# Kernel optimization log

Measured on AMD Instinct MI355X. Metric: run time of the kernel, lower is better.

The kernel has to match this reference:

```python
import jax, jax.numpy as jnp
import numpy as np

N = 100000      # num nodes
E = 1600000     # num edges (avg degree 16)
F_IN = 256      # num_node_features
HID = 128       # hid_dim
C = 16          # num_classes


def gcn_conv(x, W, b, src, dst, num_nodes):
    # Linear transform first (PyG GCNConv transforms then aggregates)
    h = x @ W  # [N, out]
    # Symmetric normalization with self-loops already included in src/dst
    ones = jnp.ones_like(dst, dtype=h.dtype)
    deg = jax.ops.segment_sum(ones, dst, num_segments=num_nodes)  # in-degree incl. self-loop
    dinv = jnp.where(deg > 0, jax.lax.rsqrt(deg), 0.0)
    norm = dinv[src] * dinv[dst]                 # [E+N]
    msg = h[src] * norm[:, None]                 # gather + scale
    out = jax.ops.segment_sum(msg, dst, num_segments=num_nodes)  # scatter-add
    return out + b


def setup_inputs() -> dict:
    key = jax.random.key(0)
    k = jax.random.split(key, 4)
    x = jax.random.normal(k[0], (N, F_IN), dtype=jnp.float32)
    edge_index = jax.random.randint(k[1], (2, E), 0, N, dtype=jnp.int32)
    W1 = jax.random.normal(k[2], (F_IN, HID), dtype=jnp.float32) * (1.0 / np.sqrt(F_IN))
    b1 = jnp.zeros((HID,), dtype=jnp.float32)
    W2 = jax.random.normal(k[3], (HID, C), dtype=jnp.float32) * (1.0 / np.sqrt(HID))
    b2 = jnp.zeros((C,), dtype=jnp.float32)
    return {"x": x, "edge_index": edge_index, "W1": W1, "b1": b1, "W2": W2, "b2": b2}


def reference(x, edge_index, W1, b1, W2, b2):
    num_nodes = x.shape[0]
    loop = jnp.arange(num_nodes, dtype=edge_index.dtype)
    src = jnp.concatenate([edge_index[0], loop])  # add self-loops
    dst = jnp.concatenate([edge_index[1], loop])
    h = gcn_conv(x, W1, b1, src, dst, num_nodes)
    h = jax.nn.relu(h)
    # F.dropout(training=self.training): identity in eval mode
    out = gcn_conv(h, W2, b2, src, dst, num_nodes)
    return out
```

## Files before the change

kernel.cpp:

```cpp
#include <hip/hip_runtime.h>
#include <cstddef>

#define CAP 48
#define NBUILD 4096

typedef short short8 __attribute__((ext_vector_type(8)));
typedef float floatx4 __attribute__((ext_vector_type(4)));

__device__ inline float b2f_lo(unsigned int u) {
  union { unsigned int i; float f; } c;
  c.i = u << 16;
  return c.f;
}
__device__ inline float b2f_hi(unsigned int u) {
  union { unsigned int i; float f; } c;
  c.i = u & 0xFFFF0000u;
  return c.f;
}
__device__ inline unsigned short f2b(float f) {
  union { float f; unsigned int i; } c;
  c.f = f;
  unsigned int u = c.i;
  unsigned int r = (u + 0x7FFFu + ((u >> 16) & 1u)) >> 16;
  return (unsigned short)r;
}
__device__ inline float dinv_of(int c) { return rsqrtf((float)(c + 1)); }

__global__ void k_prep(int* __restrict__ cnt, int N,
                       const float* __restrict__ W1, unsigned short* __restrict__ W1T) {
  int i = blockIdx.x * 256 + threadIdx.x;
  if (i < N) cnt[i] = 0;
  if (i < 256 * 128) {
    int k = i >> 7, n = i & 127;
    W1T[n * 256 + k] = f2b(W1[i]);
  }
}

__global__ __launch_bounds__(256) void k_build_gemm1(
    const int* __restrict__ src, const int* __restrict__ dst, int E, int N,
    int* __restrict__ cnt, int* __restrict__ bucket,
    const float* __restrict__ X, const unsigned short* __restrict__ W1T,
    unsigned short* __restrict__ H1, int M) {
  __shared__ unsigned short As[64 * 72];
  __shared__ unsigned short Bs[128 * 72];

  if ((int)blockIdx.x < NBUILD) {
    const int g = blockIdx.x & 7;
    const int S = (N + 7) >> 3;
    const int lo = g * S;
    const int hi = min(N, lo + S);
    const int tb = ((int)blockIdx.x >> 3) * 256 + (int)threadIdx.x;
    const int T = (NBUILD >> 3) * 256;
    const int E4 = E & ~3;

    for (int i0 = tb * 4; i0 < E4; i0 += T * 4) {
      int4 d4 = *(const int4*)(dst + i0);
      int4 s4 = *(const int4*)(src + i0);
      int p0 = CAP, p1 = CAP, p2 = CAP, p3 = CAP;
      if (d4.x >= lo && d4.x < hi) p0 = atomicAdd(&cnt[d4.x], 1);
      if (d4.y >= lo && d4.y < hi) p1 = atomicAdd(&cnt[d4.y], 1);
      if (d4.z >= lo && d4.z < hi) p2 = atomicAdd(&cnt[d4.z], 1);
      if (d4.w >= lo && d4.w < hi) p3 = atomicAdd(&cnt[d4.w], 1);
      if (p0 < CAP) bucket[(size_t)d4.x * CAP + p0] = s4.x;
      if (p1 < CAP) bucket[(size_t)d4.y * CAP + p1] = s4.y;
      if (p2 < CAP) bucket[(size_t)d4.z * CAP + p2] = s4.z;
      if (p3 < CAP) bucket[(size_t)d4.w * CAP + p3] = s4.w;
    }
    if (tb < E - E4) {
      int i = E4 + tb;
      int d = dst[i], s = src[i];
      if (d >= lo && d < hi) {
        int pos = atomicAdd(&cnt[d], 1);
        if (pos < CAP) bucket[(size_t)d * CAP + pos] = s;
      }
    }
    return;
  }

  const int bid = (int)blockIdx.x - NBUILD;
  const int tid = threadIdx.x;
  const int wave = tid >> 6;
  const int lane = tid & 63;
  const int quad = lane >> 4;
  const int l16 = lane & 15;
  const int row0 = bid * 64;
  const int n0 = wave * 32;

  floatx4 acc[4][2];
#pragma unroll
  for (int r = 0; r < 4; r++)
#pragma unroll
    for (int c = 0; c < 2; c++) acc[r][c] = (floatx4){0.f, 0.f, 0.f, 0.f};

  for (int k0 = 0; k0 < 256; k0 += 64) {
    {
      int r = tid >> 2;
      int qk = (tid & 3) * 16;
      int gr = row0 + r;
      float4 v[4];
#pragma unroll
      for (int u = 0; u < 4; u++) v[u] = make_float4(0.f, 0.f, 0.f, 0.f);
      if (gr < M) {
        const float4* xp = (const float4*)(X + (size_t)gr * 256 + k0 + qk);
#pragma unroll
        for (int u = 0; u < 4; u++) v[u] = xp[u];
      }
      unsigned short tmp[16];
#pragma unroll
      for (int u = 0; u < 4; u++) {
        tmp[u * 4 + 0] = f2b(v[u].x); tmp[u * 4 + 1] = f2b(v[u].y);
        tmp[u * 4 + 2] = f2b(v[u].z); tmp[u * 4 + 3] = f2b(v[u].w);
      }
      unsigned short* p = As + r * 72 + qk;
      *(uint4*)(p) = *(const uint4*)(tmp);
      *(uint4*)(p + 8) = *(const uint4*)(tmp + 8);
    }
    {
      int n = tid >> 1;
      int half = (tid & 1) * 32;
      const uint4* wp = (const uint4*)(W1T + (size_t)n * 256 + k0 + half);
      uint4 w0 = wp[0];
      uint4 w1 = wp[1];
      uint4 w2 = wp[2];
      uint4 w3 = wp[3];
      unsigned short* p = Bs + n * 72 + half;
      *(uint4*)(p) = w0;
      *(uint4*)(p + 8) = w1;
      *(uint4*)(p + 16) = w2;
      *(uint4*)(p + 24) = w3;
    }
    __syncthreads();

#pragma unroll
    for (int s = 0; s < 2; s++) {
      short8 afr[4], bfr[2];
#pragma unroll
      for (int r = 0; r < 4; r++)
        afr[r] = *(const short8*)(As + (r * 16 + l16) * 72 + s * 32 + quad * 8);
#pragma unroll
      for (int c = 0; c < 2; c++)
        bfr[c] = *(const short8*)(Bs + (n0 + c * 16 + l16) * 72 + s * 32 + quad * 8);
#pragma unroll
      for (int r = 0; r < 4; r++)
#pragma unroll
        for (int c = 0; c < 2; c++)
          acc[r][c] = __builtin_amdgcn_mfma_f32_16x16x32_bf16(afr[r], bfr[c], acc[r][c], 0, 0, 0);
    }
    __syncthreads();
  }

#pragma unroll
  for (int r = 0; r < 4; r++) {
#pragma unroll
    for (int c = 0; c < 2; c++) {
      int col = n0 + c * 16 + l16;
#pragma unroll
      for (int i = 0; i < 4; i++) {
        int gr = row0 + r * 16 + quad * 4 + i;
        if (gr < M) H1[(size_t)gr * 128 + col] = f2b(acc[r][c][i]);
      }
    }
  }
}

__global__ __launch_bounds__(256) void k_agg1(const unsigned short* __restrict__ H1,
                                              const int* __restrict__ cnt,
                                              const int* __restrict__ bucket,
                                              const float* __restrict__ b1,
                                              unsigned short* __restrict__ A1, int N) {
  const int lane = threadIdx.x & 15;
  const int node = blockIdx.x * 16 + (threadIdx.x >> 4);
  if (node >= N) return;
  const int cn = cnt[node];
  const float di = dinv_of(cn);
  const float wself = di * di;
  const int deg = min(cn, CAP);
  const int* bk = bucket + (size_t)node * CAP;

  int idx0 = (lane < deg) ? bk[lane] : 0;
  int idx1 = (lane + 16 < deg) ? bk[lane + 16] : 0;
  int idx2 = (lane + 32 < deg) ? bk[lane + 32] : 0;
  float dv0 = (lane < deg) ? dinv_of(cnt[idx0]) : 0.f;
  float dv1 = (lane + 16 < deg) ? dinv_of(cnt[idx1]) : 0.f;
  float dv2 = (lane + 32 < deg) ? dinv_of(cnt[idx2]) : 0.f;

  uint4 hs = ((const uint4*)(H1 + (size_t)node * 128))[lane];
  float a0 = b2f_lo(hs.x) * wself, a1 = b2f_hi(hs.x) * wself;
  float a2 = b2f_lo(hs.y) * wself, a3 = b2f_hi(hs.y) * wself;
  float a4 = b2f_lo(hs.z) * wself, a5 = b2f_hi(hs.z) * wself;
  float a6 = b2f_lo(hs.w) * wself, a7 = b2f_hi(hs.w) * wself;
  float c0 = 0.f, c1 = 0.f, c2 = 0.f, c3 = 0.f, c4 = 0.f, c5 = 0.f, c6 = 0.f, c7 = 0.f;

  for (int j = 0; j < deg; j += 4) {
    int b = j >> 4;
    int idxB = (b == 0) ? idx0 : ((b == 1) ? idx1 : idx2);
    float dvB = (b == 0) ? dv0 : ((b == 1) ? dv1 : dv2);
    int base = j & 15;
    int s0 = __shfl(idxB, base + 0, 16);
    int s1 = __shfl(idxB, base + 1, 16);
    int s2 = __shfl(idxB, base + 2, 16);
    int s3 = __shfl(idxB, base + 3, 16);
    float w0 = __shfl(dvB, base + 0, 16) * di;
    float w1 = __shfl(dvB, base + 1, 16) * di;
    float w2 = __shfl(dvB, base + 2, 16) * di;
    float w3 = __shfl(dvB, base + 3, 16) * di;
    uint4 v0 = ((const uint4*)(H1 + (size_t)s0 * 128))[lane];
    uint4 v1 = ((const uint4*)(H1 + (size_t)s1 * 128))[lane];
    uint4 v2 = ((const uint4*)(H1 + (size_t)s2 * 128))[lane];
    uint4 v3 = ((const uint4*)(H1 + (size_t)s3 * 128))[lane];
    a0 += b2f_lo(v0.x) * w0; a1 += b2f_hi(v0.x) * w0;
    a2 += b2f_lo(v0.y) * w0; a3 += b2f_hi(v0.y) * w0;
    a4 += b2f_lo(v0.z) * w0; a5 += b2f_hi(v0.z) * w0;
    a6 += b2f_lo(v0.w) * w0; a7 += b2f_hi(v0.w) * w0;
    c0 += b2f_lo(v1.x) * w1; c1 += b2f_hi(v1.x) * w1;
    c2 += b2f_lo(v1.y) * w1; c3 += b2f_hi(v1.y) * w1;
    c4 += b2f_lo(v1.z) * w1; c5 += b2f_hi(v1.z) * w1;
    c6 += b2f_lo(v1.w) * w1; c7 += b2f_hi(v1.w) * w1;
    a0 += b2f_lo(v2.x) * w2; a1 += b2f_hi(v2.x) * w2;
    a2 += b2f_lo(v2.y) * w2; a3 += b2f_hi(v2.y) * w2;
    a4 += b2f_lo(v2.z) * w2; a5 += b2f_hi(v2.z) * w2;
    a6 += b2f_lo(v2.w) * w2; a7 += b2f_hi(v2.w) * w2;
    c0 += b2f_lo(v3.x) * w3; c1 += b2f_hi(v3.x) * w3;
    c2 += b2f_lo(v3.y) * w3; c3 += b2f_hi(v3.y) * w3;
    c4 += b2f_lo(v3.z) * w3; c5 += b2f_hi(v3.z) * w3;
    c6 += b2f_lo(v3.w) * w3; c7 += b2f_hi(v3.w) * w3;
  }
  a0 += c0; a1 += c1; a2 += c2; a3 += c3;
  a4 += c4; a5 += c5; a6 += c6; a7 += c7;

  float4 bb0 = ((const float4*)b1)[lane * 2];
  float4 bb1 = ((const float4*)b1)[lane * 2 + 1];
  a0 = fmaxf(a0 + bb0.x, 0.f); a1 = fmaxf(a1 + bb0.y, 0.f);
  a2 = fmaxf(a2 + bb0.z, 0.f); a3 = fmaxf(a3 + bb0.w, 0.f);
  a4 = fmaxf(a4 + bb1.x, 0.f); a5 = fmaxf(a5 + bb1.y, 0.f);
  a6 = fmaxf(a6 + bb1.z, 0.f); a7 = fmaxf(a7 + bb1.w, 0.f);
  uint4 o;
  o.x = (unsigned int)f2b(a0) | ((unsigned int)f2b(a1) << 16);
  o.y = (unsigned int)f2b(a2) | ((unsigned int)f2b(a3) << 16);
  o.z = (unsigned int)f2b(a4) | ((unsigned int)f2b(a5) << 16);
  o.w = (unsigned int)f2b(a6) | ((unsigned int)f2b(a7) << 16);
  ((uint4*)(A1 + (size_t)node * 128))[lane] = o;
}

__global__ __launch_bounds__(256) void k_gemm2(const unsigned short* __restrict__ A1,
                                               const float* __restrict__ W2,
                                               unsigned short* __restrict__ H2, int M) {
  __shared__ float Ws[128 * 16];
  int tid = threadIdx.x;
  ((float4*)Ws)[tid] = ((const float4*)W2)[tid];
  ((float4*)Ws)[tid + 256] = ((const float4*)W2)[tid + 256];
  __syncthreads();
  int q = tid & 3;
  int row = blockIdx.x * 64 + (tid >> 2);
  if (row >= M) return;
  float4 acc = make_float4(0.f, 0.f, 0.f, 0.f);
  const unsigned short* arow = A1 + (size_t)row * 128;
  for (int k0 = 0; k0 < 128; k0 += 8) {
    uint4 av = *(const uint4*)(arow + k0);
    float a[8];
    a[0] = b2f_lo(av.x); a[1] = b2f_hi(av.x);
    a[2] = b2f_lo(av.y); a[3] = b2f_hi(av.y);
    a[4] = b2f_lo(av.z); a[5] = b2f_hi(av.z);
    a[6] = b2f_lo(av.w); a[7] = b2f_hi(av.w);
#pragma unroll
    for (int kk = 0; kk < 8; kk++) {
      float4 wv = *(const float4*)&Ws[(k0 + kk) * 16 + q * 4];
      acc.x += a[kk] * wv.x; acc.y += a[kk] * wv.y;
      acc.z += a[kk] * wv.z; acc.w += a[kk] * wv.w;
    }
  }
  ushort4 o;
  o.x = f2b(acc.x); o.y = f2b(acc.y); o.z = f2b(acc.z); o.w = f2b(acc.w);
  ((ushort4*)(H2 + (size_t)row * 16))[q] = o;
}

__global__ __launch_bounds__(256) void k_agg2(const unsigned short* __restrict__ H2,
                                              const int* __restrict__ cnt,
                                              const int* __restrict__ bucket,
                                              const float* __restrict__ b2,
                                              float* __restrict__ out, int N) {
  const int half = threadIdx.x & 1;
  const int node = blockIdx.x * 128 + (threadIdx.x >> 1);
  if (node >= N) return;
  const int cn = cnt[node];
  const float di = dinv_of(cn);
  const float wself = di * di;
  const int deg = min(cn, CAP);
  const int* bk = bucket + (size_t)node * CAP;

  uint4 h = ((const uint4*)(H2 + (size_t)node * 16))[half];
  float a0 = b2f_lo(h.x) * wself, a1 = b2f_hi(h.x) * wself;
  float a2 = b2f_lo(h.y) * wself, a3 = b2f_hi(h.y) * wself;
  float a4 = b2f_lo(h.z) * wself, a5 = b2f_hi(h.z) * wself;
  float a6 = b2f_lo(h.w) * wself, a7 = b2f_hi(h.w) * wself;

  for (int j = 0; j < deg; j += 4) {
    int4 s4 = *(const int4*)(bk + j);
    int s0 = s4.x;
    int s1 = (j + 1 < deg) ? s4.y : 0;
    int s2 = (j + 2 < deg) ? s4.z : 0;
    int s3 = (j + 3 < deg) ? s4.w : 0;
    float w0 = dinv_of(cnt[s0]) * di;
    float w1 = (j + 1 < deg) ? dinv_of(cnt[s1]) * di : 0.f;
    float w2 = (j + 2 < deg) ? dinv_of(cnt[s2]) * di : 0.f;
    float w3 = (j + 3 < deg) ? dinv_of(cnt[s3]) * di : 0.f;
    uint4 v0 = ((const uint4*)(H2 + (size_t)s0 * 16))[half];
    uint4 v1 = ((const uint4*)(H2 + (size_t)s1 * 16))[half];
    uint4 v2 = ((const uint4*)(H2 + (size_t)s2 * 16))[half];
    uint4 v3 = ((const uint4*)(H2 + (size_t)s3 * 16))[half];
    a0 += b2f_lo(v0.x) * w0 + b2f_lo(v1.x) * w1 + b2f_lo(v2.x) * w2 + b2f_lo(v3.x) * w3;
    a1 += b2f_hi(v0.x) * w0 + b2f_hi(v1.x) * w1 + b2f_hi(v2.x) * w2 + b2f_hi(v3.x) * w3;
    a2 += b2f_lo(v0.y) * w0 + b2f_lo(v1.y) * w1 + b2f_lo(v2.y) * w2 + b2f_lo(v3.y) * w3;
    a3 += b2f_hi(v0.y) * w0 + b2f_hi(v1.y) * w1 + b2f_hi(v2.y) * w2 + b2f_hi(v3.y) * w3;
    a4 += b2f_lo(v0.z) * w0 + b2f_lo(v1.z) * w1 + b2f_lo(v2.z) * w2 + b2f_lo(v3.z) * w3;
    a5 += b2f_hi(v0.z) * w0 + b2f_hi(v1.z) * w1 + b2f_hi(v2.z) * w2 + b2f_hi(v3.z) * w3;
    a6 += b2f_lo(v0.w) * w0 + b2f_lo(v1.w) * w1 + b2f_lo(v2.w) * w2 + b2f_lo(v3.w) * w3;
    a7 += b2f_hi(v0.w) * w0 + b2f_hi(v1.w) * w1 + b2f_hi(v2.w) * w2 + b2f_hi(v3.w) * w3;
  }

  float4 bb0 = ((const float4*)b2)[half * 2];
  float4 bb1 = ((const float4*)b2)[half * 2 + 1];
  float4 o0 = make_float4(a0 + bb0.x, a1 + bb0.y, a2 + bb0.z, a3 + bb0.w);
  float4 o1 = make_float4(a4 + bb1.x, a5 + bb1.y, a6 + bb1.z, a7 + bb1.w);
  ((float4*)(out + (size_t)node * 16))[half * 2] = o0;
  ((float4*)(out + (size_t)node * 16))[half * 2 + 1] = o1;
}


extern "C" void kernel_launch(void* const* d_in, const int* in_sizes, int n_in,
                              void* d_out, int out_size, void* d_ws, size_t ws_size,
                              hipStream_t stream) {
  const float* x  = (const float*)d_in[0];
  const int* eidx = (const int*)d_in[1];
  const float* W1 = (const float*)d_in[2];
  const float* b1 = (const float*)d_in[3];
  const float* W2 = (const float*)d_in[4];
  const float* b2 = (const float*)d_in[5];
  float* out = (float*)d_out;

  const int HID = in_sizes[3];
  const int F   = in_sizes[2] / HID;
  const int N   = in_sizes[0] / F;
  const int E   = in_sizes[1] / 2;
  (void)n_in; (void)out_size; (void)ws_size;

  const int* src = eidx;
  const int* dst = eidx + E;

  char* base = (char*)d_ws;
  size_t off = 0;
  auto alloc = [&](size_t bytes) -> char* {
    char* p = base + off;
    off = (off + bytes + 255) & ~(size_t)255;
    return p;
  };
  int*            cnt    = (int*)alloc((size_t)N * 4);
  int*            bucket = (int*)alloc((size_t)N * CAP * 4);
  unsigned short* w1t    = (unsigned short*)alloc((size_t)256 * 128 * 2);
  unsigned short* h1     = (unsigned short*)alloc((size_t)N * 128 * 2);
  unsigned short* a1     = (unsigned short*)alloc((size_t)N * 128 * 2);
  unsigned short* h2     = (unsigned short*)alloc((size_t)N * 16 * 2);

  const int nbN = (N + 255) / 256;
  const int gblocks = (N + 63) / 64;

  hipLaunchKernelGGL(k_prep, dim3(nbN), dim3(256), 0, stream, cnt, N, W1, w1t);
  hipLaunchKernelGGL(k_build_gemm1, dim3(NBUILD + gblocks), dim3(256), 0, stream,
                     src, dst, E, N, cnt, bucket, x, w1t, h1, N);
  hipLaunchKernelGGL(k_agg1, dim3((N + 15) / 16), dim3(256), 0, stream, h1, cnt, bucket,
                     b1, a1, N);
  hipLaunchKernelGGL(k_gemm2, dim3((N + 63) / 64), dim3(256), 0, stream, a1, W2, h2, N);
  hipLaunchKernelGGL(k_agg2, dim3((N + 127) / 128), dim3(256), 0, stream, h2, cnt, bucket,
                     b2, out, N);
}
```

Baseline: 345.4 us.

## Interleave build and GEMM blocks in fused launch, shrink GEMM K-tile to 32

Block indices of the fused edge-bucketing and GEMM1 kernel are now spread evenly between build work and GEMM tiles, using a proportional mapping instead of putting all build blocks first. This lets the atomic-heavy scatter and the compute/bandwidth-bound GEMM run at the same time on the device. The GEMM K step is also cut from 64 to 32, which halves shared memory per block and may raise occupancy, at the cost of twice as many barrier-separated iterations.

```diff
diff --git a/kernel.cpp b/kernel.cpp
--- a/kernel.cpp
+++ b/kernel.cpp
@@ -40,16 +40,22 @@
     const int* __restrict__ src, const int* __restrict__ dst, int E, int N,
     int* __restrict__ cnt, int* __restrict__ bucket,
     const float* __restrict__ X, const unsigned short* __restrict__ W1T,
-    unsigned short* __restrict__ H1, int M) {
-  __shared__ unsigned short As[64 * 72];
-  __shared__ unsigned short Bs[128 * 72];
-
-  if ((int)blockIdx.x < NBUILD) {
-    const int g = blockIdx.x & 7;
+    unsigned short* __restrict__ H1, int M, int gblocks, int total) {
+  __shared__ unsigned short As[64 * 40];
+  __shared__ unsigned short Bs[128 * 40];
+
+  const unsigned int idx = blockIdx.x;
+  const unsigned int gBefore = (idx * (unsigned int)gblocks) / (unsigned int)total;
+  const unsigned int gAfter = ((idx + 1) * (unsigned int)gblocks) / (unsigned int)total;
+  const bool isGemm = (gAfter > gBefore);
+
+  if (!isGemm) {
+    const int bi = (int)(idx - gBefore);
+    const int g = bi & 7;
     const int S = (N + 7) >> 3;
     const int lo = g * S;
     const int hi = min(N, lo + S);
-    const int tb = ((int)blockIdx.x >> 3) * 256 + (int)threadIdx.x;
+    const int tb = (bi >> 3) * 256 + (int)threadIdx.x;
     const int T = (NBUILD >> 3) * 256;
     const int E4 = E & ~3;
 
@@ -77,7 +83,7 @@
     return;
   }
 
-  const int bid = (int)blockIdx.x - NBUILD;
+  const int bid = (int)gBefore;
   const int tid = threadIdx.x;
   const int wave = tid >> 6;
   const int lane = tid & 63;
@@ -92,60 +98,46 @@
 #pragma unroll
     for (int c = 0; c < 2; c++) acc[r][c] = (floatx4){0.f, 0.f, 0.f, 0.f};
 
-  for (int k0 = 0; k0 < 256; k0 += 64) {
+  for (int k0 = 0; k0 < 256; k0 += 32) {
     {
       int r = tid >> 2;
-      int qk = (tid & 3) * 16;
+      int q = tid & 3;
       int gr = row0 + r;
-      float4 v[4];
-#pragma unroll
-      for (int u = 0; u < 4; u++) v[u] = make_float4(0.f, 0.f, 0.f, 0.f);
+      float4 v0 = make_float4(0.f, 0.f, 0.f, 0.f), v1 = v0;
       if (gr < M) {
-        const float4* xp = (const float4*)(X + (size_t)gr * 256 + k0 + qk);
-#pragma unroll
-        for (int u = 0; u < 4; u++) v[u] = xp[u];
+        const float4* xp = (const float4*)(X + (size_t)gr * 256 + k0 + q * 8);
+        v0 = xp[0];
+        v1 = xp[1];
       }
-      unsigned short tmp[16];
-#pragma unroll
-      for (int u = 0; u < 4; u++) {
-        tmp[u * 4 + 0] = f2b(v[u].x); tmp[u * 4 + 1] = f2b(v[u].y);
-        tmp[u * 4 + 2] = f2b(v[u].z); tmp[u * 4 + 3] = f2b(v[u].w);
-      }
-      unsigned short* p = As + r * 72 + qk;
-      *(uint4*)(p) = *(const uint4*)(tmp);
-      *(uint4*)(p + 8) = *(const uint4*)(tmp + 8);
+      unsigned short tmp[8];
+      tmp[0] = f2b(v0.x); tmp[1] = f2b(v0.y); tmp[2] = f2b(v0.z); tmp[3] = f2b(v0.w);
+      tmp[4] = f2b(v1.x); tmp[5] = f2b(v1.y); tmp[6] = f2b(v1.z); tmp[7] = f2b(v1.w);
+      *(uint4*)(As + r * 40 + q * 8) = *(const uint4*)(tmp);
     }
     {
       int n = tid >> 1;
-      int half = (tid & 1) * 32;
+      int half = (tid & 1) * 16;
       const uint4* wp = (const uint4*)(W1T + (size_t)n * 256 + k0 + half);
       uint4 w0 = wp[0];
       uint4 w1 = wp[1];
-      uint4 w2 = wp[2];
-      uint4 w3 = wp[3];
-      unsigned short* p = Bs + n * 72 + half;
+      unsigned short* p = Bs + n * 40 + half;
       *(uint4*)(p) = w0;
       *(uint4*)(p + 8) = w1;
-      *(uint4*)(p + 16) = w2;
-      *(uint4*)(p + 24) = w3;
     }
     __syncthreads();
 
-#pragma unroll
-    for (int s = 0; s < 2; s++) {
-      short8 afr[4], bfr[2];
-#pragma unroll
-      for (int r = 0; r < 4; r++)
-        afr[r] = *(const short8*)(As + (r * 16 + l16) * 72 + s * 32 + quad * 8);
+    short8 afr[4], bfr[2];
+#pragma unroll
+    for (int r = 0; r < 4; r++)
+      afr[r] = *(const short8*)(As + (r * 16 + l16) * 40 + quad * 8);
+#pragma unroll
+    for (int c = 0; c < 2; c++)
+      bfr[c] = *(const short8*)(Bs + (n0 + c * 16 + l16) * 40 + quad * 8);
+#pragma unroll
+    for (int r = 0; r < 4; r++)
 #pragma unroll
       for (int c = 0; c < 2; c++)
-        bfr[c] = *(const short8*)(Bs + (n0 + c * 16 + l16) * 72 + s * 32 + quad * 8);
-#pragma unroll
-      for (int r = 0; r < 4; r++)
-#pragma unroll
-        for (int c = 0; c < 2; c++)
-          acc[r][c] = __builtin_amdgcn_mfma_f32_16x16x32_bf16(afr[r], bfr[c], acc[r][c], 0, 0, 0);
-    }
+        acc[r][c] = __builtin_amdgcn_mfma_f32_16x16x32_bf16(afr[r], bfr[c], acc[r][c], 0, 0, 0);
     __syncthreads();
   }
 
@@ -363,10 +355,11 @@
 
   const int nbN = (N + 255) / 256;
   const int gblocks = (N + 63) / 64;
+  const int total = NBUILD + gblocks;
 
   hipLaunchKernelGGL(k_prep, dim3(nbN), dim3(256), 0, stream, cnt, N, W1, w1t);
-  hipLaunchKernelGGL(k_build_gemm1, dim3(NBUILD + gblocks), dim3(256), 0, stream,
-                     src, dst, E, N, cnt, bucket, x, w1t, h1, N);
+  hipLaunchKernelGGL(k_build_gemm1, dim3(total), dim3(256), 0, stream,
+                     src, dst, E, N, cnt, bucket, x, w1t, h1, N, gblocks, total);
   hipLaunchKernelGGL(k_agg1, dim3((N + 15) / 16), dim3(256), 0, stream, h1, cnt, bucket,
                      b1, a1, N);
   hipLaunchKernelGGL(k_gemm2, dim3((N + 63) / 64), dim3(256), 0, stream, a1, W2, h2, N);
```

Measured after the change: 339.6 us. No clear change (-1.7%).
